# Optimization experiments

Measured on AMD Instinct MI355X. Metric: run time of the kernel, lower is better.

Reference implementation:

```python
import jax, jax.numpy as jnp
import numpy as np

N_BOND = 2_000_000
N_ATOM = 100_000
N_STRUCT = 2
THREEBODY_CUTOFF = 0.8


def setup_inputs() -> dict:
    key = jax.random.key(0)
    k1, k2 = jax.random.split(key)
    # bonds grouped (sorted) by source atom, as _compute_threebody assumes
    bond_src = jnp.sort(jax.random.randint(k1, (N_BOND,), 0, N_ATOM))
    bond_length = jax.random.uniform(k2, (N_BOND,), dtype=jnp.float32)
    n_atoms = jnp.full((N_STRUCT,), N_ATOM // N_STRUCT, dtype=jnp.int32)
    return {"bond_src": bond_src, "bond_length": bond_length, "n_atoms": n_atoms}


def reference(bond_src, bond_length, n_atoms):
    """Vectorized equivalent of compute_threebody_indices.

    Returns (bond_indices [T,2] pairs of ORIGINAL bond ids, n_triple_ij [n_bond],
    n_triple_i [n_atom], n_triple_s [n_struct]). Replaces the O(n) Python loops
    with segment-sum (degree count), prefix-sum (CSR offsets) and a flat
    enumeration of ordered within-atom bond pairs (j != k).
    """
    n_bond = bond_src.shape[0]
    n_atom = int(jnp.sum(n_atoms))
    n_struct = n_atoms.shape[0]

    # --- filter bonds by three-body cutoff, remember original bond ids ---
    mask = bond_length <= THREEBODY_CUTOFF
    kept = jnp.nonzero(mask)[0]          # original bond indices of surviving bonds
    src = bond_src[kept]                 # still sorted (subset of a sorted array)

    # --- per-atom bond counts and CSR offsets (parallel histogram + scan) ---
    deg = jax.ops.segment_sum(jnp.ones_like(src), src, num_segments=n_atom)
    bond_offset = jnp.cumsum(deg) - deg  # start of each atom's bond block

    # --- triples per atom / per bond / per structure ---
    n_triple_i = deg * (deg - 1)
    T = int(jnp.sum(n_triple_i))

    # --- enumerate all ordered pairs (j, k), j != k, within each atom block ---
    tri_atom = jnp.repeat(jnp.arange(n_atom), n_triple_i, total_repeat_length=T)
    tri_start = (jnp.cumsum(n_triple_i) - n_triple_i)[tri_atom]
    t = jnp.arange(T) - tri_start        # local triple index in [0, d*(d-1))
    d = deg[tri_atom]                    # d >= 2 wherever triples exist
    j = t // (d - 1)
    kp = t % (d - 1)
    k = kp + (kp >= j).astype(kp.dtype)  # skip k == j, preserving loop order
    b0 = bond_offset[tri_atom] + j       # relative (filtered) bond index
    b1 = bond_offset[tri_atom] + k
    bond_indices = jnp.stack([kept[b0], kept[b1]], axis=1)  # back to ORIGINAL ids

    # angles per ORIGINAL bond: deg(src)-1 for surviving bonds, 0 for filtered
    n_triple_ij = jnp.zeros(n_bond, dtype=deg.dtype).at[kept].set(deg[src] - 1)

    # angles per structure
    struct_id = jnp.repeat(jnp.arange(n_struct), n_atoms, total_repeat_length=n_atom)
    n_triple_s = jax.ops.segment_sum(n_triple_i, struct_id, num_segments=n_struct)

    return bond_indices, n_triple_ij, n_triple_i, n_triple_s
```

## Files before the change

kernel.cpp:

```cpp
#include <hip/hip_runtime.h>


#define CUTOFF 0.8f
#define NATOM_C 100000
#define TPB 1024
#define WIN 64

__global__ void k0_init(int* wstart, int* wend, int n_atom) {
    int i = blockIdx.x * blockDim.x + threadIdx.x;
    if (i < n_atom) { wstart[i] = 0; wend[i] = 0; }
}

__global__ void k1_bounds(const int* __restrict__ src, int* wstart, int* wend, int n_bond) {
    int i = blockIdx.x * blockDim.x + threadIdx.x;
    if (i >= n_bond) return;
    int a = src[i];
    if (i == 0 || src[i - 1] != a) wstart[a] = i;
    if (i == n_bond - 1 || src[i + 1] != a) wend[a] = i + 1;
}

__global__ void sA_reduce(const float* __restrict__ len, int* __restrict__ bsums, int n) {
    __shared__ int tmp[256];
    int t = threadIdx.x;
    int base = blockIdx.x * TPB + t * 4;
    int s = 0;
    #pragma unroll
    for (int i = 0; i < 4; i++) {
        int idx = base + i;
        if (idx < n) s += (len[idx] <= CUTOFF) ? 1 : 0;
    }
    tmp[t] = s;
    __syncthreads();
    for (int off = 128; off > 0; off >>= 1) {
        if (t < off) tmp[t] += tmp[t + off];
        __syncthreads();
    }
    if (t == 0) bsums[blockIdx.x] = tmp[0];
}

__global__ void s_scan1(int* __restrict__ arr, int n, int* __restrict__ total) {
    const int B = 256;
    __shared__ int sums[B];
    int t = threadIdx.x;
    int chunk = (n + B - 1) / B;
    int lo = t * chunk; if (lo > n) lo = n;
    int hi = lo + chunk; if (hi > n) hi = n;
    int ssum = 0;
    for (int i = lo; i < hi; i++) ssum += arr[i];
    sums[t] = ssum;
    __syncthreads();
    for (int off = 1; off < B; off <<= 1) {
        int v = (t >= off) ? sums[t - off] : 0;
        __syncthreads();
        sums[t] += v;
        __syncthreads();
    }
    int run = sums[t] - ssum;
    for (int i = lo; i < hi; i++) { int v = arr[i]; arr[i] = run; run += v; }
    if (t == B - 1) *total = sums[B - 1];
}

__global__ void sC_emit(const float* __restrict__ len, const int* __restrict__ pA,
                        int* __restrict__ msk_scan, int* __restrict__ ckept, int n) {
    __shared__ int tmp[256];
    int t = threadIdx.x;
    int base = blockIdx.x * TPB + t * 4;
    int m[4]; int s = 0;
    #pragma unroll
    for (int i = 0; i < 4; i++) {
        int idx = base + i;
        m[i] = (idx < n && len[idx] <= CUTOFF) ? 1 : 0;
        s += m[i];
    }
    tmp[t] = s;
    __syncthreads();
    for (int off = 1; off < 256; off <<= 1) {
        int v = (t >= off) ? tmp[t - off] : 0;
        __syncthreads();
        tmp[t] += v;
        __syncthreads();
    }
    int run = tmp[t] - s + pA[blockIdx.x];
    #pragma unroll
    for (int i = 0; i < 4; i++) {
        int idx = base + i;
        if (idx < n) {
            msk_scan[idx] = run;
            if (m[i]) { ckept[run] = idx; run++; }
        }
    }
}

__global__ void k4_atom(const int* __restrict__ wstart, const int* __restrict__ wend,
                        const int* __restrict__ msk_scan, int* __restrict__ deg,
                        int* __restrict__ bo, int* __restrict__ out_i, int n_atom) {
    int a = blockIdx.x * blockDim.x + threadIdx.x;
    if (a >= n_atom) return;
    int s = wstart[a], e = wend[a];
    int b = msk_scan[s];
    int d = msk_scan[e] - b;
    deg[a] = d; bo[a] = b; out_i[a] = d * (d - 1);
}

__global__ void sD_partial(const int* __restrict__ vals, int* __restrict__ exsc,
                           int* __restrict__ bsums, int n) {
    __shared__ int tmp[256];
    int t = threadIdx.x;
    int base = blockIdx.x * TPB + t * 4;
    int v[4]; int s = 0;
    #pragma unroll
    for (int i = 0; i < 4; i++) {
        int idx = base + i;
        v[i] = (idx < n) ? vals[idx] : 0;
        s += v[i];
    }
    tmp[t] = s;
    __syncthreads();
    for (int off = 1; off < 256; off <<= 1) {
        int x = (t >= off) ? tmp[t - off] : 0;
        __syncthreads();
        tmp[t] += x;
        __syncthreads();
    }
    int run = tmp[t] - s;
    #pragma unroll
    for (int i = 0; i < 4; i++) {
        int idx = base + i;
        if (idx < n) exsc[idx] = run;
        run += v[i];
    }
    if (t == 255) bsums[blockIdx.x] = tmp[255];
}

__global__ void kFinal(const int* __restrict__ exsc, const int* __restrict__ pB,
                       const int* __restrict__ totalT, int* __restrict__ tstart,
                       int* __restrict__ block_atom,
                       const int* __restrict__ n_atoms_arr, int* __restrict__ out_s,
                       int n_atom, int n_struct) {
    int a = blockIdx.x * blockDim.x + threadIdx.x;
    int T = *totalT;
    if (a < n_atom) {
        int ts  = exsc[a] + pB[a >> 10];
        tstart[a] = ts;
        int ts1 = (a + 1 < n_atom) ? (exsc[a + 1] + pB[(a + 1) >> 10]) : T;
        if (a == 0) tstart[n_atom] = T;
        for (int b = (ts + TPB - 1) / TPB; b * TPB < ts1; b++) block_atom[b] = a;
    }
    if (a < n_struct) {
        int off = 0;
        for (int s2 = 0; s2 < a; s2++) off += n_atoms_arr[s2];
        int c = n_atoms_arr[a];
        int x0 = off, x1 = off + c;
        int t0 = (x0 < n_atom) ? (exsc[x0] + pB[x0 >> 10]) : T;
        int t1 = (x1 < n_atom) ? (exsc[x1] + pB[x1 >> 10]) : T;
        out_s[a] = t1 - t0;
    }
}

__global__ void kT_triples(const int* __restrict__ tstart, const int* __restrict__ bo,
                           const int* __restrict__ deg, const int* __restrict__ ckept,
                           const int* __restrict__ block_atom,
                           int2* __restrict__ out_pairs, int n_atom, int T) {
    __shared__ int s_ts[WIN + 1];
    __shared__ int s_bo[WIN];
    __shared__ int s_dm1[WIN];
    int tid = threadIdx.x;
    int a0 = block_atom[blockIdx.x];
    for (int i = tid; i <= WIN; i += 256) {
        int ai = a0 + i; if (ai > n_atom) ai = n_atom;
        s_ts[i] = tstart[ai];
    }
    for (int i = tid; i < WIN; i += 256) {
        int ai = a0 + i; if (ai > n_atom - 1) ai = n_atom - 1;
        s_bo[i] = bo[ai];
        s_dm1[i] = deg[ai] - 1;
    }
    __syncthreads();
    int t = blockIdx.x * TPB + tid;
    int a_off = 0;
    #pragma unroll
    for (int it = 0; it < TPB / 256; it++, t += 256) {
        if (t >= T) return;
        while (a_off < WIN && t >= s_ts[a_off + 1]) a_off++;
        int tp, dm1, bof;
        if (a_off < WIN) {
            tp = t - s_ts[a_off]; dm1 = s_dm1[a_off]; bof = s_bo[a_off];
        } else {
            int a = a0 + WIN;
            while (a + 1 <= n_atom && t >= tstart[a + 1]) a++;
            tp = t - tstart[a]; dm1 = deg[a] - 1; bof = bo[a];
        }
        float r = 1.0f / (float)dm1;
        int j = (int)((float)tp * r);
        int rem = tp - j * dm1;
        if (rem < 0)         { j -= 1; rem += dm1; }
        else if (rem >= dm1) { j += 1; rem -= dm1; }
        int k = rem + ((rem >= j) ? 1 : 0);
        out_pairs[t] = make_int2(ckept[bof + j], ckept[bof + k]);
    }
}

__global__ void kIJ(const int* __restrict__ src, const float* __restrict__ len,
                    const int* __restrict__ deg, int* __restrict__ out_ij, int n_bond) {
    int i = blockIdx.x * blockDim.x + threadIdx.x;
    if (i >= n_bond) return;
    out_ij[i] = (len[i] <= CUTOFF) ? (deg[src[i]] - 1) : 0;
}

extern "C" void kernel_launch(void* const* d_in, const int* in_sizes, int n_in,
                              void* d_out, int out_size, void* d_ws, size_t ws_size,
                              hipStream_t stream) {
    const int*   bond_src    = (const int*)d_in[0];
    const float* bond_len    = (const float*)d_in[1];
    const int*   n_atoms_arr = (const int*)d_in[2];
    int n_bond   = in_sizes[0];
    int n_struct = in_sizes[2];
    const int n_atom = NATOM_C;
    int T2 = out_size - n_bond - n_atom - n_struct;
    int T  = T2 / 2;

    int nblkA = (n_bond + TPB - 1) / TPB;
    int nblkD = (n_atom + TPB - 1) / TPB;
    int nblkT = (T + TPB - 1) / TPB;

    int* ws         = (int*)d_ws;
    int* wstart     = ws;                       ws += n_atom;
    int* wend       = ws;                       ws += n_atom;
    int* deg        = ws;                       ws += n_atom;
    int* bo         = ws;                       ws += n_atom;
    int* tstart     = ws;                       ws += n_atom + 1;
    int* exscD      = ws;                       ws += n_atom;
    int* pA         = ws;                       ws += nblkA;
    int* pB         = ws;                       ws += nblkD;
    int* totalT     = ws;                       ws += 1;
    int* msk_scan   = ws;                       ws += n_bond + 1;
    int* ckept      = ws;                       ws += n_bond;
    int* block_atom = ws;                       ws += (nblkT > 0 ? nblkT : 1);

    int*  out       = (int*)d_out;
    int2* out_pairs = (int2*)out;
    int*  out_ij    = out + T2;
    int*  out_i     = out_ij + n_bond;
    int*  out_s     = out_i + n_atom;

    k0_init   <<<(n_atom + 255) / 256, 256, 0, stream>>>(wstart, wend, n_atom);
    k1_bounds <<<(n_bond + 255) / 256, 256, 0, stream>>>(bond_src, wstart, wend, n_bond);
    sA_reduce <<<nblkA, 256, 0, stream>>>(bond_len, pA, n_bond);
    s_scan1   <<<1, 256, 0, stream>>>(pA, nblkA, msk_scan + n_bond);
    sC_emit   <<<nblkA, 256, 0, stream>>>(bond_len, pA, msk_scan, ckept, n_bond);
    k4_atom   <<<(n_atom + 255) / 256, 256, 0, stream>>>(wstart, wend, msk_scan, deg, bo, out_i, n_atom);
    sD_partial<<<nblkD, 256, 0, stream>>>(out_i, exscD, pB, n_atom);
    s_scan1   <<<1, 256, 0, stream>>>(pB, nblkD, totalT);
    kFinal    <<<(n_atom + 255) / 256, 256, 0, stream>>>(exscD, pB, totalT, tstart, block_atom,
                                                         n_atoms_arr, out_s, n_atom, n_struct);
    if (nblkT > 0)
        kT_triples<<<nblkT, 256, 0, stream>>>(tstart, bo, deg, ckept, block_atom,
                                              out_pairs, n_atom, T);
    kIJ       <<<(n_bond + 255) / 256, 256, 0, stream>>>(bond_src, bond_len, deg, out_ij, n_bond);
}
```

Baseline: 293.9 us.

## Restructure pipeline: atomic degree count, fuse out_ij into emit, two triples per thread

Per-atom degrees are now built with run-compressed atomicAdds inside the mask-count pass, which replaces the init and boundary kernels and the full msk_scan array. The per-bond out_ij output is written inside the compaction kernel, so the separate kIJ pass goes away. The bond-offset and triple-offset scans are computed together in one dual scan. The triples kernel now gives each thread two consecutive triples and writes them as one int4 store, with twice as many triples per block. The aims are fewer launches, fewer full-array passes and wider stores, at the cost of atomic contention and more lookup work per thread.

```diff
diff --git a/kernel.cpp b/kernel.cpp
--- a/kernel.cpp
+++ b/kernel.cpp
@@ -4,38 +4,48 @@
 #define CUTOFF 0.8f
 #define NATOM_C 100000
 #define TPB 1024
+#define TPB2 2048
 #define WIN 64
 
-__global__ void k0_init(int* wstart, int* wend, int n_atom) {
+__global__ void kZ(int* __restrict__ deg, int n_atom) {
     int i = blockIdx.x * blockDim.x + threadIdx.x;
-    if (i < n_atom) { wstart[i] = 0; wend[i] = 0; }
-}
-
-__global__ void k1_bounds(const int* __restrict__ src, int* wstart, int* wend, int n_bond) {
-    int i = blockIdx.x * blockDim.x + threadIdx.x;
-    if (i >= n_bond) return;
-    int a = src[i];
-    if (i == 0 || src[i - 1] != a) wstart[a] = i;
-    if (i == n_bond - 1 || src[i + 1] != a) wend[a] = i + 1;
-}
-
-__global__ void sA_reduce(const float* __restrict__ len, int* __restrict__ bsums, int n) {
+    if (i < n_atom) deg[i] = 0;
+}
+
+__global__ void s1_maskdeg(const float* __restrict__ len, const int* __restrict__ src,
+                           int* __restrict__ pA, int* __restrict__ deg, int n) {
     __shared__ int tmp[256];
     int t = threadIdx.x;
     int base = blockIdx.x * TPB + t * 4;
-    int s = 0;
-    #pragma unroll
-    for (int i = 0; i < 4; i++) {
-        int idx = base + i;
-        if (idx < n) s += (len[idx] <= CUTOFF) ? 1 : 0;
-    }
+    int m[4], sv[4];
+    if (base + 3 < n) {
+        float4 L = *(const float4*)(len + base);
+        int4   S = *(const int4*)(src + base);
+        m[0] = L.x <= CUTOFF; m[1] = L.y <= CUTOFF; m[2] = L.z <= CUTOFF; m[3] = L.w <= CUTOFF;
+        sv[0] = S.x; sv[1] = S.y; sv[2] = S.z; sv[3] = S.w;
+    } else {
+        #pragma unroll
+        for (int i = 0; i < 4; i++) {
+            int idx = base + i;
+            m[i]  = (idx < n) && (len[idx] <= CUTOFF);
+            sv[i] = (idx < n) ? src[idx] : -1;
+        }
+    }
+    int s = m[0] + m[1] + m[2] + m[3];
+    int cur = sv[0], cnt = m[0];
+    #pragma unroll
+    for (int i = 1; i < 4; i++) {
+        if (sv[i] == cur) cnt += m[i];
+        else { if (cnt) atomicAdd(&deg[cur], cnt); cur = sv[i]; cnt = m[i]; }
+    }
+    if (cnt) atomicAdd(&deg[cur], cnt);
     tmp[t] = s;
     __syncthreads();
     for (int off = 128; off > 0; off >>= 1) {
         if (t < off) tmp[t] += tmp[t + off];
         __syncthreads();
     }
-    if (t == 0) bsums[blockIdx.x] = tmp[0];
+    if (t == 0) pA[blockIdx.x] = tmp[0];
 }
 
 __global__ void s_scan1(int* __restrict__ arr, int n, int* __restrict__ total) {
@@ -60,18 +70,27 @@
     if (t == B - 1) *total = sums[B - 1];
 }
 
-__global__ void sC_emit(const float* __restrict__ len, const int* __restrict__ pA,
-                        int* __restrict__ msk_scan, int* __restrict__ ckept, int n) {
+__global__ void s3_emit(const float* __restrict__ len, const int* __restrict__ src,
+                        const int* __restrict__ pA, const int* __restrict__ deg,
+                        int* __restrict__ ckept, int* __restrict__ out_ij, int n) {
     __shared__ int tmp[256];
     int t = threadIdx.x;
     int base = blockIdx.x * TPB + t * 4;
-    int m[4]; int s = 0;
-    #pragma unroll
-    for (int i = 0; i < 4; i++) {
-        int idx = base + i;
-        m[i] = (idx < n && len[idx] <= CUTOFF) ? 1 : 0;
-        s += m[i];
-    }
+    int m[4], sv[4];
+    if (base + 3 < n) {
+        float4 L = *(const float4*)(len + base);
+        int4   S = *(const int4*)(src + base);
+        m[0] = L.x <= CUTOFF; m[1] = L.y <= CUTOFF; m[2] = L.z <= CUTOFF; m[3] = L.w <= CUTOFF;
+        sv[0] = S.x; sv[1] = S.y; sv[2] = S.z; sv[3] = S.w;
+    } else {
+        #pragma unroll
+        for (int i = 0; i < 4; i++) {
+            int idx = base + i;
+            m[i]  = (idx < n) && (len[idx] <= CUTOFF);
+            sv[i] = (idx < n) ? src[idx] : 0;
+        }
+    }
+    int s = m[0] + m[1] + m[2] + m[3];
     tmp[t] = s;
     __syncthreads();
     for (int off = 1; off < 256; off <<= 1) {
@@ -85,82 +104,121 @@
     for (int i = 0; i < 4; i++) {
         int idx = base + i;
         if (idx < n) {
-            msk_scan[idx] = run;
+            out_ij[idx] = m[i] ? (deg[sv[i]] - 1) : 0;
             if (m[i]) { ckept[run] = idx; run++; }
         }
     }
 }
 
-__global__ void k4_atom(const int* __restrict__ wstart, const int* __restrict__ wend,
-                        const int* __restrict__ msk_scan, int* __restrict__ deg,
-                        int* __restrict__ bo, int* __restrict__ out_i, int n_atom) {
-    int a = blockIdx.x * blockDim.x + threadIdx.x;
-    if (a >= n_atom) return;
-    int s = wstart[a], e = wend[a];
-    int b = msk_scan[s];
-    int d = msk_scan[e] - b;
-    deg[a] = d; bo[a] = b; out_i[a] = d * (d - 1);
-}
-
-__global__ void sD_partial(const int* __restrict__ vals, int* __restrict__ exsc,
-                           int* __restrict__ bsums, int n) {
-    __shared__ int tmp[256];
+__global__ void s4_atomscan(const int* __restrict__ deg, int* __restrict__ out_i,
+                            int* __restrict__ exB, int* __restrict__ exT,
+                            int* __restrict__ pBB, int* __restrict__ pBT, int n) {
+    __shared__ int shB[256];
+    __shared__ int shT[256];
     int t = threadIdx.x;
     int base = blockIdx.x * TPB + t * 4;
-    int v[4]; int s = 0;
+    int d[4], tr[4];
     #pragma unroll
     for (int i = 0; i < 4; i++) {
         int idx = base + i;
-        v[i] = (idx < n) ? vals[idx] : 0;
-        s += v[i];
-    }
-    tmp[t] = s;
+        d[i]  = (idx < n) ? deg[idx] : 0;
+        tr[i] = d[i] * (d[i] - 1);
+        if (idx < n) out_i[idx] = tr[i];
+    }
+    int sB = d[0] + d[1] + d[2] + d[3];
+    int sT = tr[0] + tr[1] + tr[2] + tr[3];
+    shB[t] = sB; shT[t] = sT;
     __syncthreads();
     for (int off = 1; off < 256; off <<= 1) {
-        int x = (t >= off) ? tmp[t - off] : 0;
-        __syncthreads();
-        tmp[t] += x;
-        __syncthreads();
-    }
-    int run = tmp[t] - s;
+        int vB = (t >= off) ? shB[t - off] : 0;
+        int vT = (t >= off) ? shT[t - off] : 0;
+        __syncthreads();
+        shB[t] += vB; shT[t] += vT;
+        __syncthreads();
+    }
+    int runB = shB[t] - sB, runT = shT[t] - sT;
     #pragma unroll
     for (int i = 0; i < 4; i++) {
         int idx = base + i;
-        if (idx < n) exsc[idx] = run;
-        run += v[i];
-    }
-    if (t == 255) bsums[blockIdx.x] = tmp[255];
-}
-
-__global__ void kFinal(const int* __restrict__ exsc, const int* __restrict__ pB,
-                       const int* __restrict__ totalT, int* __restrict__ tstart,
-                       int* __restrict__ block_atom,
-                       const int* __restrict__ n_atoms_arr, int* __restrict__ out_s,
-                       int n_atom, int n_struct) {
+        if (idx < n) { exB[idx] = runB; exT[idx] = runT; }
+        runB += d[i]; runT += tr[i];
+    }
+    if (t == 255) { pBB[blockIdx.x] = shB[255]; pBT[blockIdx.x] = shT[255]; }
+}
+
+__global__ void s5_dual(int* __restrict__ pBB, int* __restrict__ pBT, int n,
+                        int* __restrict__ totT) {
+    const int B = 256;
+    __shared__ int sB[B];
+    __shared__ int sT[B];
+    int t = threadIdx.x;
+    int chunk = (n + B - 1) / B;
+    int lo = t * chunk; if (lo > n) lo = n;
+    int hi = lo + chunk; if (hi > n) hi = n;
+    int ssB = 0, ssT = 0;
+    for (int i = lo; i < hi; i++) { ssB += pBB[i]; ssT += pBT[i]; }
+    sB[t] = ssB; sT[t] = ssT;
+    __syncthreads();
+    for (int off = 1; off < B; off <<= 1) {
+        int vB = (t >= off) ? sB[t - off] : 0;
+        int vT = (t >= off) ? sT[t - off] : 0;
+        __syncthreads();
+        sB[t] += vB; sT[t] += vT;
+        __syncthreads();
+    }
+    int runB = sB[t] - ssB, runT = sT[t] - ssT;
+    for (int i = lo; i < hi; i++) {
+        int vB = pBB[i], vT = pBT[i];
+        pBB[i] = runB; pBT[i] = runT;
+        runB += vB; runT += vT;
+    }
+    if (t == B - 1) *totT = sT[B - 1];
+}
+
+__global__ void s6_final(const int* __restrict__ exB, const int* __restrict__ exT,
+                         const int* __restrict__ pBB, const int* __restrict__ pBT,
+                         const int* __restrict__ totT, int* __restrict__ bo,
+                         int* __restrict__ tstart, int* __restrict__ block_atom,
+                         const int* __restrict__ n_atoms_arr, int* __restrict__ out_s,
+                         int n_atom, int n_struct) {
     int a = blockIdx.x * blockDim.x + threadIdx.x;
-    int T = *totalT;
+    int T = *totT;
     if (a < n_atom) {
-        int ts  = exsc[a] + pB[a >> 10];
+        bo[a] = exB[a] + pBB[a >> 10];
+        int ts = exT[a] + pBT[a >> 10];
         tstart[a] = ts;
-        int ts1 = (a + 1 < n_atom) ? (exsc[a + 1] + pB[(a + 1) >> 10]) : T;
+        int ts1 = (a + 1 < n_atom) ? (exT[a + 1] + pBT[(a + 1) >> 10]) : T;
         if (a == 0) tstart[n_atom] = T;
-        for (int b = (ts + TPB - 1) / TPB; b * TPB < ts1; b++) block_atom[b] = a;
+        for (int b = (ts + TPB2 - 1) / TPB2; b * TPB2 < ts1; b++) block_atom[b] = a;
     }
     if (a < n_struct) {
         int off = 0;
         for (int s2 = 0; s2 < a; s2++) off += n_atoms_arr[s2];
         int c = n_atoms_arr[a];
         int x0 = off, x1 = off + c;
-        int t0 = (x0 < n_atom) ? (exsc[x0] + pB[x0 >> 10]) : T;
-        int t1 = (x1 < n_atom) ? (exsc[x1] + pB[x1 >> 10]) : T;
+        int t0 = (x0 < n_atom) ? (exT[x0] + pBT[x0 >> 10]) : T;
+        int t1 = (x1 < n_atom) ? (exT[x1] + pBT[x1 >> 10]) : T;
         out_s[a] = t1 - t0;
     }
 }
 
-__global__ void kT_triples(const int* __restrict__ tstart, const int* __restrict__ bo,
+__device__ __forceinline__ void triple_pair(int tp, int dm1, int bof,
+                                            const int* __restrict__ ckept,
+                                            int& x, int& y) {
+    float r = 1.0f / (float)dm1;
+    int j = (int)((float)tp * r);
+    int rem = tp - j * dm1;
+    if (rem < 0)         { j -= 1; rem += dm1; }
+    else if (rem >= dm1) { j += 1; rem -= dm1; }
+    int k = rem + ((rem >= j) ? 1 : 0);
+    x = ckept[bof + j];
+    y = ckept[bof + k];
+}
+
+__global__ void s7_triples(const int* __restrict__ tstart, const int* __restrict__ bo,
                            const int* __restrict__ deg, const int* __restrict__ ckept,
                            const int* __restrict__ block_atom,
-                           int2* __restrict__ out_pairs, int n_atom, int T) {
+                           int4* __restrict__ out4, int n_atom, int T) {
     __shared__ int s_ts[WIN + 1];
     __shared__ int s_bo[WIN];
     __shared__ int s_dm1[WIN];
@@ -171,40 +229,36 @@
         s_ts[i] = tstart[ai];
     }
     for (int i = tid; i < WIN; i += 256) {
-        int ai = a0 + i; if (ai > n_atom - 1) ai = n_atom - 1;
-        s_bo[i] = bo[ai];
+        int ai = a0 + i; if (ai >= n_atom) ai = n_atom - 1;
+        s_bo[i]  = bo[ai];
         s_dm1[i] = deg[ai] - 1;
     }
     __syncthreads();
-    int t = blockIdx.x * TPB + tid;
     int a_off = 0;
     #pragma unroll
-    for (int it = 0; it < TPB / 256; it++, t += 256) {
-        if (t >= T) return;
-        while (a_off < WIN && t >= s_ts[a_off + 1]) a_off++;
-        int tp, dm1, bof;
+    for (int it = 0; it < TPB2 / 512; it++) {
+        int t0 = blockIdx.x * TPB2 + it * 512 + tid * 2;
+        if (t0 >= T) return;
+        while (a_off < WIN && t0 >= s_ts[a_off + 1]) a_off++;
+        int x0, y0, x1, y1;
         if (a_off < WIN) {
-            tp = t - s_ts[a_off]; dm1 = s_dm1[a_off]; bof = s_bo[a_off];
+            triple_pair(t0 - s_ts[a_off], s_dm1[a_off], s_bo[a_off], ckept, x0, y0);
         } else {
             int a = a0 + WIN;
-            while (a + 1 <= n_atom && t >= tstart[a + 1]) a++;
-            tp = t - tstart[a]; dm1 = deg[a] - 1; bof = bo[a];
-        }
-        float r = 1.0f / (float)dm1;
-        int j = (int)((float)tp * r);
-        int rem = tp - j * dm1;
-        if (rem < 0)         { j -= 1; rem += dm1; }
-        else if (rem >= dm1) { j += 1; rem -= dm1; }
-        int k = rem + ((rem >= j) ? 1 : 0);
-        out_pairs[t] = make_int2(ckept[bof + j], ckept[bof + k]);
-    }
-}
-
-__global__ void kIJ(const int* __restrict__ src, const float* __restrict__ len,
-                    const int* __restrict__ deg, int* __restrict__ out_ij, int n_bond) {
-    int i = blockIdx.x * blockDim.x + threadIdx.x;
-    if (i >= n_bond) return;
-    out_ij[i] = (len[i] <= CUTOFF) ? (deg[src[i]] - 1) : 0;
+            while (a + 1 <= n_atom && t0 >= tstart[a + 1]) a++;
+            triple_pair(t0 - tstart[a], deg[a] - 1, bo[a], ckept, x0, y0);
+        }
+        int a1 = a_off;
+        while (a1 < WIN && t0 + 1 >= s_ts[a1 + 1]) a1++;
+        if (a1 < WIN) {
+            triple_pair(t0 + 1 - s_ts[a1], s_dm1[a1], s_bo[a1], ckept, x1, y1);
+        } else {
+            int a = a0 + WIN;
+            while (a + 1 <= n_atom && t0 + 1 >= tstart[a + 1]) a++;
+            triple_pair(t0 + 1 - tstart[a], deg[a] - 1, bo[a], ckept, x1, y1);
+        }
+        out4[t0 >> 1] = make_int4(x0, y0, x1, y1);
+    }
 }
 
 extern "C" void kernel_launch(void* const* d_in, const int* in_sizes, int n_in,
@@ -221,40 +275,38 @@
 
     int nblkA = (n_bond + TPB - 1) / TPB;
     int nblkD = (n_atom + TPB - 1) / TPB;
-    int nblkT = (T + TPB - 1) / TPB;
+    int nblkT = (T + TPB2 - 1) / TPB2;
 
     int* ws         = (int*)d_ws;
-    int* wstart     = ws;                       ws += n_atom;
-    int* wend       = ws;                       ws += n_atom;
-    int* deg        = ws;                       ws += n_atom;
-    int* bo         = ws;                       ws += n_atom;
-    int* tstart     = ws;                       ws += n_atom + 1;
-    int* exscD      = ws;                       ws += n_atom;
-    int* pA         = ws;                       ws += nblkA;
-    int* pB         = ws;                       ws += nblkD;
-    int* totalT     = ws;                       ws += 1;
-    int* msk_scan   = ws;                       ws += n_bond + 1;
-    int* ckept      = ws;                       ws += n_bond;
-    int* block_atom = ws;                       ws += (nblkT > 0 ? nblkT : 1);
+    int* deg        = ws;              ws += n_atom;
+    int* bo         = ws;              ws += n_atom;
+    int* tstart     = ws;              ws += n_atom + 1;
+    int* exB        = ws;              ws += n_atom;
+    int* exT        = ws;              ws += n_atom;
+    int* pA         = ws;              ws += nblkA;
+    int* pBB        = ws;              ws += nblkD;
+    int* pBT        = ws;              ws += nblkD;
+    int* totT       = ws;              ws += 1;
+    int* keptTot    = ws;              ws += 1;
+    int* ckept      = ws;              ws += n_bond;
+    int* block_atom = ws;              ws += (nblkT > 0 ? nblkT : 1);
 
     int*  out       = (int*)d_out;
-    int2* out_pairs = (int2*)out;
+    int4* out4      = (int4*)out;
     int*  out_ij    = out + T2;
     int*  out_i     = out_ij + n_bond;
     int*  out_s     = out_i + n_atom;
 
-    k0_init   <<<(n_atom + 255) / 256, 256, 0, stream>>>(wstart, wend, n_atom);
-    k1_bounds <<<(n_bond + 255) / 256, 256, 0, stream>>>(bond_src, wstart, wend, n_bond);
-    sA_reduce <<<nblkA, 256, 0, stream>>>(bond_len, pA, n_bond);
-    s_scan1   <<<1, 256, 0, stream>>>(pA, nblkA, msk_scan + n_bond);
-    sC_emit   <<<nblkA, 256, 0, stream>>>(bond_len, pA, msk_scan, ckept, n_bond);
-    k4_atom   <<<(n_atom + 255) / 256, 256, 0, stream>>>(wstart, wend, msk_scan, deg, bo, out_i, n_atom);
-    sD_partial<<<nblkD, 256, 0, stream>>>(out_i, exscD, pB, n_atom);
-    s_scan1   <<<1, 256, 0, stream>>>(pB, nblkD, totalT);
-    kFinal    <<<(n_atom + 255) / 256, 256, 0, stream>>>(exscD, pB, totalT, tstart, block_atom,
-                                                         n_atoms_arr, out_s, n_atom, n_struct);
+    kZ        <<<(n_atom + 255) / 256, 256, 0, stream>>>(deg, n_atom);
+    s1_maskdeg<<<nblkA, 256, 0, stream>>>(bond_len, bond_src, pA, deg, n_bond);
+    s_scan1   <<<1, 256, 0, stream>>>(pA, nblkA, keptTot);
+    s3_emit   <<<nblkA, 256, 0, stream>>>(bond_len, bond_src, pA, deg, ckept, out_ij, n_bond);
+    s4_atomscan<<<nblkD, 256, 0, stream>>>(deg, out_i, exB, exT, pBB, pBT, n_atom);
+    s5_dual   <<<1, 256, 0, stream>>>(pBB, pBT, nblkD, totT);
+    s6_final  <<<(n_atom + 255) / 256, 256, 0, stream>>>(exB, exT, pBB, pBT, totT, bo, tstart,
+                                                         block_atom, n_atoms_arr, out_s,
+                                                         n_atom, n_struct);
     if (nblkT > 0)
-        kT_triples<<<nblkT, 256, 0, stream>>>(tstart, bo, deg, ckept, block_atom,
-                                              out_pairs, n_atom, T);
-    kIJ       <<<(n_bond + 255) / 256, 256, 0, stream>>>(bond_src, bond_len, deg, out_ij, n_bond);
-}
+        s7_triples<<<nblkT, 256, 0, stream>>>(tstart, bo, deg, ckept, block_atom,
+                                              out4, n_atom, T);
+}
```

New measurement: 276.8 us. 5.8% less time.
